# Optimization experiments

Hardware: AMD Instinct MI355X
Metric: run time of the kernel (lower is better)

The kernel has to match this reference:

```python
import jax, jax.numpy as jnp
import numpy as np
import math

B = 2048
INPUT_SIZE = 1024
OUTPUT_SIZE = 512
SPONGE = 1024
ACT = 256
REC = 256
STORE = ACT + REC  # 512
DEPTH = 8
BDEPTH = 10
NEUTRAL_C = 1.0
SQRT2 = math.sqrt(2.0)


def _make_structure():
    # Deterministic stand-in for the module's random.sample-based recall wiring.
    rng = np.random.RandomState(0)
    half = (SPONGE + 1) // 2
    shuffle_perm = np.array([i // 2 + (i % 2) * half for i in range(SPONGE)], dtype=np.int64)
    unused = []
    recall = []
    for i in range(DEPTH):
        unused.extend(range(i * STORE, (i + 1) * STORE))
        sel = rng.choice(len(unused), size=REC, replace=False)
        sel_set = set(sel.tolist())
        recall.append([unused[k] for k in sorted(sel_set)])
        unused = [u for k, u in enumerate(unused) if k not in sel_set]
    out_mem = np.array(sorted(unused), dtype=np.int64)  # 2048 leftover memory columns
    bf_size = len(out_mem) + SPONGE  # 3072
    bf_depth = int(math.ceil(math.log2(bf_size)))  # 12
    bf_half = (bf_size + 1) // 2
    bf_perm = np.array([i // 2 + (i % 2) * bf_half for i in range(bf_size)], dtype=np.int64)
    return shuffle_perm, np.array(recall, dtype=np.int64), out_mem, bf_perm, bf_size, bf_depth


def setup_inputs() -> dict:
    key = jax.random.key(0)
    ks = jax.random.split(key, 6)
    shuffle_perm, recall_idx, out_mem_idx, bf_perm, bf_size, bf_depth = _make_structure()
    return {
        "X": jax.random.normal(ks[0], (B, INPUT_SIZE), jnp.float32),
        "scales": jnp.ones((INPUT_SIZE,), jnp.float32),
        "angles": jax.random.uniform(ks[1], (DEPTH, BDEPTH, SPONGE // 2), jnp.float32) * (2 * math.pi),
        "act_bias": jax.random.normal(ks[2], (DEPTH, ACT), jnp.float32),
        "act_activation": jax.random.normal(ks[3], (DEPTH, ACT), jnp.float32),
        "act_curvature": jax.random.normal(ks[4], (DEPTH, ACT), jnp.float32),
        "bf_angles": jax.random.uniform(ks[5], (bf_depth, bf_size // 2), jnp.float32) * (2 * math.pi),
        "shuffle_perm": jnp.asarray(shuffle_perm),
        "recall_idx": jnp.asarray(recall_idx),
        "output_mem_idx": jnp.asarray(out_mem_idx),
        "bf_perm": jnp.asarray(bf_perm),
    }


def _base_activation(x, c):
    # In the source, `a` is overwritten with torch.tensor(1.0), so a == 1.
    t = (math.pi / 4) / c
    y0 = (1.0 / c) * (1.0 / SQRT2 - math.cos(math.pi / 2))  # = 1/(c*sqrt(2))
    m0 = math.sin(math.pi / 2)  # = 1
    y1 = (1.0 / c) * (1.0 / SQRT2 - 1.0)
    m1 = math.sin(0.0)  # = 0
    mid = (1.0 / c) * (1.0 / SQRT2 - jnp.cos(math.pi / 4 + c * x))
    return jnp.where(x > t, y0 + m0 * (x - t), jnp.where(x < -t, y1 + m1 * (x + t), mid))


def _butterfly(x, angles, perm):
    # angles: [n_layers, exch]; shuffle -> Givens rotation per pair, extra passthrough
    exch = angles.shape[1]
    for j in range(angles.shape[0]):
        s = x[:, perm]
        x1, x2 = s[:, :exch], s[:, exch:2 * exch]
        ca, sa = jnp.cos(angles[j]), jnp.sin(angles[j])
        x = jnp.concatenate([ca * x1 + sa * x2, -sa * x1 + ca * x2, s[:, 2 * exch:]], axis=1)
    return x


def reference(X, scales, angles, act_bias, act_activation, act_curvature, bf_angles,
              shuffle_perm, recall_idx, output_mem_idx, bf_perm):
    Xs = X * scales
    sponge = Xs[:, :SPONGE]  # input_size == sponge_size: no zero pad, memory[0] is empty
    mem = jnp.zeros((Xs.shape[0], DEPTH * STORE), Xs.dtype)
    for i in range(DEPTH):
        sponge = _butterfly(sponge, angles[i], shuffle_perm)
        x1 = sponge[:, STORE:STORE + ACT] + act_bias[i]  # activation_position == store_size
        c = 0.5 * NEUTRAL_C * (act_curvature[i] + jnp.sqrt(act_curvature[i] ** 2 + 1.0))
        ap = _base_activation(x1, c)
        am = _base_activation(-x1, c)
        act_out = jnp.stack([ap, am], axis=2).reshape(ap.shape[0], 2 * ACT)  # interleave +/-
        mem = mem.at[:, i * STORE:(i + 1) * STORE].set(sponge[:, :STORE])
        recall = mem[:, recall_idx[i]]  # indices only address already-filled columns
        # [act_out | sponge[store:act_pos] (empty) | sponge[act_pos+ACT:] | recall]
        sponge = jnp.concatenate([act_out, sponge[:, STORE + ACT:], recall], axis=1)
    pre = jnp.concatenate([mem[:, output_mem_idx], sponge], axis=1)  # [B, 3072]
    out = _butterfly(pre, bf_angles, bf_perm)
    return out[:, :OUTPUT_SIZE]
```

## Files before the change

### kernel.cpp

```cpp
#include <hip/hip_runtime.h>
#include <math.h>

#define NB 2048
#define DEPTH 8

#define FTAB_OFF    0
#define BF01_OFF    81920
#define BFF_OFF     88064
#define ACT4_OFF    98304
#define PHYSA_OFF   106496
#define PHYSR_OFF   110592
#define PHYSO2_OFF  112640

#define MB0 2304
#define MB1 3328

#define SBAR() asm volatile("s_waitcnt lgkmcnt(0)\n\ts_barrier" ::: "memory")

__global__ void setup_kernel(const float* __restrict__ angles,
                             const float* __restrict__ bf_angles,
                             const float* __restrict__ act_bias,
                             const float* __restrict__ act_curv,
                             const int* __restrict__ recall_idx,
                             const int* __restrict__ out_mem_idx,
                             float* __restrict__ ws) {
    __shared__ int physL[4096];
    __shared__ int rcl[2048];
    __shared__ int oml[2048];
    if (blockIdx.x < 200) {
        int id = blockIdx.x * 256 + threadIdx.x;
        if (id < 40960) {
            int w = id & 3, t = (id >> 2) & 255, dg = id >> 10;
            int d = dg / 5, g = dg - 5 * d;
            int a = 2 * (t & 127) + (t >> 7);
            int pair = (w == 0) ? a : (w == 1) ? (a + 256)
                     : (w == 2) ? (2 * a) : (2 * a + 1);
            int st = 2 * g + (w >> 1);
            float ang = angles[(d * 10 + st) * 512 + pair];
            float s, c; __sincosf(ang, &s, &c);
            ws[FTAB_OFF + 2 * id]     = c;
            ws[FTAB_OFF + 2 * id + 1] = s;
        } else if (id < 44032) {
            int e = id - 40960;
            int w = e & 3; int ti = e >> 2;
            int t = ti / 3; int i = ti - 3 * t;
            int a = t + 256 * i;
            int pair = (w == 0) ? a : (w == 1) ? (a + 768)
                     : (w == 2) ? (2 * a) : (2 * a + 1);
            int stage = (w < 2) ? 0 : 1;
            float ang = bf_angles[stage * 1536 + pair];
            float s, c; __sincosf(ang, &s, &c);
            ws[BF01_OFF + 2 * e]     = c;
            ws[BF01_OFF + 2 * e + 1] = s;
        } else if (id < 49152) {
            int e = id - 44032;
            int f = e >> 10; int rem = e & 1023; int t = rem >> 2; int w = rem & 3;
            int P;
            if (f == 0) P = 3 * t;
            else if (f < 4) { int k = 8 - 2 * f;
                              P = ((t >> (2 * f)) * (768 >> k)) + (t & ((256 >> k) - 1)); }
            else P = t;
            int pair = (w == 0) ? P : (w == 1) ? (P + 768)
                     : (w == 2) ? (2 * P) : (2 * P + 1);
            int stage = (w < 2) ? (2 + 2 * f) : (3 + 2 * f);
            float ang = bf_angles[stage * 1536 + pair];
            float s, c; __sincosf(ang, &s, &c);
            ws[BFF_OFF + 2 * e]     = c;
            ws[BFF_OFF + 2 * e + 1] = s;
        } else if (id < 51200) {
            int ida = id - 49152;
            float cu = act_curv[ida];
            float c  = 0.5f * (cu + sqrtf(cu * cu + 1.0f));
            ((float4*)(ws + ACT4_OFF))[ida] =
                make_float4(act_bias[ida], c, 1.0f / c, 0.0f);
        }
    } else {
        int tid = threadIdx.x;
        for (int e = tid; e < 2048; e += 256) rcl[e] = recall_idx[e];
        for (int e = tid; e < 2048; e += 256) oml[e] = out_mem_idx[e];
        for (int e = tid; e < 512; e += 256) physL[e] = e;
        __syncthreads();
        for (int d = 1; d < 8; ++d) {
            for (int j = tid; j < 512; j += 256) {
                int p;
                if (j < 256) p = 256 + d * 256 + j;
                else          p = physL[rcl[(d - 1) * 256 + (j - 256)]];
                physL[512 * d + j] = p;
            }
            __syncthreads();
        }
        int* pa = (int*)(ws + PHYSA_OFF);
        for (int e = tid; e < 2048; e += 256) {
            int d = e >> 8, t = e & 255;
            int a = 2 * (t & 127) + (t >> 7);
            pa[2 * e]     = physL[d * 512 + 2 * a];
            pa[2 * e + 1] = physL[d * 512 + 2 * a + 1];
        }
        int* pr = (int*)(ws + PHYSR_OFF);
        for (int e = tid; e < 2048; e += 256)
            pr[e] = physL[rcl[e]];
        int* po = (int*)(ws + PHYSO2_OFF);
        for (int e = tid; e < 3072; e += 256) {
            int tt = e / 12; int r = e - 12 * tt; int i = r >> 2; int k = r & 3;
            int a = tt + 256 * i;
            int tl2 = a >> 1, th2 = a & 1;
            int pos = tl2 + 1536 * th2 + 384 * k;
            po[e] = (pos < 2048) ? physL[oml[pos]]
                                 : MB0 + (pos - 2048);
        }
    }
}

__device__ __forceinline__ float actf(float x, float c, float ic) {
    const float is2 = 0.70710678118654752f;
    float tt = 0.78539816339744831f * ic;
    float y0 = is2 * ic;
    float y1 = (is2 - 1.0f) * ic;
    float mid = ic * (is2 - __cosf(0.78539816339744831f + c * x));
    return x > tt ? (y0 + (x - tt)) : (x < -tt ? y1 : mid);
}

__launch_bounds__(256, 8)
__global__ void sponge_kernel(const float* __restrict__ X,
                              const float* __restrict__ scales,
                              const float* __restrict__ ws,
                              float* __restrict__ out) {
    __shared__ float L[4352];
    const int t = threadIdx.x;
    const int row = blockIdx.x;

    const float4* bf01  = (const float4*)(ws + BF01_OFF);
    const float4* bff   = (const float4*)(ws + BFF_OFF);
    const float4* act4  = (const float4*)(ws + ACT4_OFF);
    const int2* physA  = (const int2*)(ws + PHYSA_OFF);
    const int*  physr  = (const int*)(ws + PHYSR_OFF);
    const int*  physo2 = (const int*)(ws + PHYSO2_OFF);

    const int tl = t & 127, th = t >> 7;
    const int b  = tl + th * 512;
    const int a  = 2 * tl + th;
    const int Wn = 2 * (tl & 15) + 32 * th + 64 * (tl >> 4);
    const int Rn = (tl & 1) + 2 * ((tl >> 2) & 15) + 32 * ((tl >> 1) & 1)
                 + 64 * (tl >> 6) + 512 * th;
    const int u  = t - 128;

    float h0, h1, h2, h3;
    {
        const float* Xr = X + (size_t)row * 1024;
        h0 = Xr[b]       * scales[b];
        h1 = Xr[b + 128] * scales[b + 128];
        h2 = Xr[b + 256] * scales[b + 256];
        h3 = Xr[b + 384] * scales[b + 384];
    }

    int woff = MB0, roff = MB1;
    const float4* ft = (const float4*)(ws + FTAB_OFF) + 2 * t;
    float4 csA = ft[0], csB = ft[1];

#define DQUAD(cA, cB, i0, i1, i2, i3, F0, F1, F2, F3)                    \
    { float g0 =  (cA).x * (i0) + (cA).y * (i2);                         \
      float g2 = -(cA).y * (i0) + (cA).x * (i2);                         \
      float g1 =  (cA).z * (i1) + (cA).w * (i3);                         \
      float g3 = -(cA).w * (i1) + (cA).z * (i3);                         \
      F0 =  (cB).x * g0 + (cB).y * g1;                                   \
      F2 = -(cB).y * g0 + (cB).x * g1;                                   \
      F1 =  (cB).z * g2 + (cB).w * g3;                                   \
      F3 = -(cB).w * g2 + (cB).z * g3; }

    for (int d = 0; d < DEPTH; ++d) {
        for (int g = 0; g < 5; ++g) {
            float f0, f1, f2, f3;
            DQUAD(csA, csB, h0, h1, h2, h3, f0, f1, f2, f3);
            if (g < 4) {
                *(float2*)(L + woff + Wn)       = make_float2(f0, f1);
                *(float2*)(L + woff + Wn + 512) = make_float2(f2, f3);
                { int tmp = woff; woff = roff; roff = tmp; }
                ft += 512;
                float4 nA = ft[0], nB = ft[1];
                SBAR();
                h0 = L[roff + Rn];
                h1 = L[roff + Rn + 128];
                h2 = L[roff + Rn + 256];
                h3 = L[roff + Rn + 384];
                csA = nA; csB = nB;
            } else {
                int2 pm = physA[d * 256 + t];
                L[pm.x] = f0;
                L[pm.y] = f1;
                *(float2*)(L + woff + 2 * a) = make_float2(f2, f3);
                { int tmp = woff; woff = roff; roff = tmp; }
                ft += 512;
                float4 nA = ft[0], nB = ft[1];
                int r0 = 0, r1 = 0;
                float4 a0, a1, a2, a3;
                if (t < 128) {
                    int k0 = t >> 1;
                    a0 = act4[d * 256 + k0];
                    a1 = act4[d * 256 + k0 + 64];
                    a2 = act4[d * 256 + k0 + 128];
                    a3 = act4[d * 256 + k0 + 192];
                } else {
                    r0 = physr[d * 256 + u];
                    r1 = physr[d * 256 + u + 128];
                }
                SBAR();
                const float* Z = L + roff;
                if (t < 128) {
                    int k0 = t >> 1;
                    float sgn = (t & 1) ? -1.0f : 1.0f;
                    float z0 = Z[k0];
                    float z1 = Z[k0 + 64];
                    float z2 = Z[k0 + 128];
                    float z3 = Z[k0 + 192];
                    h0 = actf(sgn * (z0 + a0.x), a0.y, a0.z);
                    h1 = actf(sgn * (z1 + a1.x), a1.y, a1.z);
                    h2 = actf(sgn * (z2 + a2.x), a2.y, a2.z);
                    h3 = actf(sgn * (z3 + a3.x), a3.y, a3.z);
                } else {
                    h0 = Z[256 + u];
                    h1 = Z[384 + u];
                    h2 = L[r0];
                    h3 = L[r1];
                }
                csA = nA; csB = nB;
            }
        }
    }

    int4 pg0, pg1, pg2;
    {
        const int4* pgp = (const int4*)(physo2 + t * 12);
        pg0 = pgp[0]; pg1 = pgp[1]; pg2 = pgp[2];
    }
    L[MB0 + b]       = h0;
    L[MB0 + b + 128] = h1;
    L[MB0 + b + 256] = h2;
    L[MB0 + b + 384] = h3;
    SBAR();

    float w0, w1, w2, w3, w4, w5, w6, w7, w8, w9, w10, w11;
    w0 = L[pg0.x]; w1 = L[pg0.y]; w2 = L[pg0.z]; w3 = L[pg0.w];
    w4 = L[pg1.x]; w5 = L[pg1.y]; w6 = L[pg1.z]; w7 = L[pg1.w];
    w8 = L[pg2.x]; w9 = L[pg2.y]; w10 = L[pg2.z]; w11 = L[pg2.w];
    SBAR();

#define BF01_STEP(i, q0, q1, q2, q3)                                     \
    {                                                                    \
        float4 c01 = bf01[(t * 3 + (i)) * 2];                            \
        float4 c23 = bf01[(t * 3 + (i)) * 2 + 1];                        \
        float y0, y1, y2, y3;                                            \
        DQUAD(c01, c23, q0, q1, q2, q3, y0, y1, y2, y3);                 \
        *(float2*)(L + 2 * t + 512 * (i))        = make_float2(y0, y1);  \
        *(float2*)(L + 2 * t + 512 * (i) + 1536) = make_float2(y2, y3);  \
    }
    BF01_STEP(0, w0, w1, w2, w3)
    BF01_STEP(1, w4, w5, w6, w7)
    BF01_STEP(2, w8, w9, w10, w11)
#undef BF01_STEP
    SBAR();

#pragma unroll
    for (int f = 0; f < 4; ++f) {
        int P;
        if (f == 0) P = 3 * t;
        else { const int k = 8 - 2 * f;
               P = ((t >> (2 * f)) * (768 >> k)) + (t & ((256 >> k) - 1)); }
        int base = (P >> 1) + (P & 1) * 1536;
        float4 csS = bff[(f * 256 + t) * 2];
        float4 csT = bff[(f * 256 + t) * 2 + 1];
        float x1p = L[base];
        float x1q = L[base + 384];
        float x2p = L[base + 768];
        float x2q = L[base + 1152];
        float o1P =  csS.x * x1p + csS.y * x2p;
        float o2P = -csS.y * x1p + csS.x * x2p;
        float o1Q =  csS.z * x1q + csS.w * x2q;
        float o2Q = -csS.w * x1q + csS.z * x2q;
        float y0 =  csT.x * o1P + csT.y * o1Q;
        float y2 = -csT.y * o1P + csT.x * o1Q;
        float y1 =  csT.z * o2P + csT.w * o2Q;
        float y3 = -csT.w * o2P + csT.z * o2Q;
        SBAR();
        *(float2*)(L + 2 * P)        = make_float2(y0, y1);
        *(float2*)(L + 2 * P + 1536) = make_float2(y2, y3);
        SBAR();
    }

    {
        int base = (t >> 1) + (t & 1) * 1536;
        float4 csS = bff[(4 * 256 + t) * 2];
        float4 csT = bff[(4 * 256 + t) * 2 + 1];
        float x1p = L[base];
        float x1q = L[base + 384];
        float x2p = L[base + 768];
        float x2q = L[base + 1152];
        float o1P =  csS.x * x1p + csS.y * x2p;
        float o2P = -csS.y * x1p + csS.x * x2p;
        float o1Q =  csS.z * x1q + csS.w * x2q;
        float o2Q = -csS.w * x1q + csS.z * x2q;
        *(float2*)(out + (size_t)row * 512 + 2 * t) =
            make_float2(csT.x * o1P + csT.y * o1Q, csT.z * o2P + csT.w * o2Q);
    }
#undef DQUAD
}

extern "C" void kernel_launch(void* const* d_in, const int* in_sizes, int n_in,
                              void* d_out, int out_size, void* d_ws, size_t ws_size,
                              hipStream_t stream) {
    const float* X          = (const float*)d_in[0];
    const float* scales     = (const float*)d_in[1];
    const float* angles     = (const float*)d_in[2];
    const float* act_bias   = (const float*)d_in[3];
    const float* act_curv   = (const float*)d_in[5];
    const float* bf_angles  = (const float*)d_in[6];
    const int*   recall_idx  = (const int*)d_in[8];
    const int*   out_mem_idx = (const int*)d_in[9];

    float* ws = (float*)d_ws;

    setup_kernel<<<201, 256, 0, stream>>>(angles, bf_angles, act_bias, act_curv,
                                          recall_idx, out_mem_idx, ws);
    sponge_kernel<<<NB, 256, 0, stream>>>(X, scales, ws, (float*)d_out);
}
```

Measured before the change: 123.5 us.

## Halve threads per row and give each thread two butterfly quads

```diff
diff --git a/kernel.cpp b/kernel.cpp
--- a/kernel.cpp
+++ b/kernel.cpp
@@ -12,8 +12,8 @@
 #define PHYSR_OFF   110592
 #define PHYSO2_OFF  112640
 
-#define MB0 2304
-#define MB1 3328
+#define EXB  2304
+#define EXB1 3328
 
 #define SBAR() asm volatile("s_waitcnt lgkmcnt(0)\n\ts_barrier" ::: "memory")
 
@@ -106,7 +106,7 @@
             int tl2 = a >> 1, th2 = a & 1;
             int pos = tl2 + 1536 * th2 + 384 * k;
             po[e] = (pos < 2048) ? physL[oml[pos]]
-                                 : MB0 + (pos - 2048);
+                                 : EXB + (pos - 2048);
         }
     }
 }
@@ -120,7 +120,7 @@
     return x > tt ? (y0 + (x - tt)) : (x < -tt ? y1 : mid);
 }
 
-__launch_bounds__(256, 8)
+__launch_bounds__(128, 4)
 __global__ void sponge_kernel(const float* __restrict__ X,
                               const float* __restrict__ scales,
                               const float* __restrict__ ws,
@@ -136,26 +136,19 @@
     const int*  physr  = (const int*)(ws + PHYSR_OFF);
     const int*  physo2 = (const int*)(ws + PHYSO2_OFF);
 
-    const int tl = t & 127, th = t >> 7;
-    const int b  = tl + th * 512;
-    const int a  = 2 * tl + th;
-    const int Wn = 2 * (tl & 15) + 32 * th + 64 * (tl >> 4);
-    const int Rn = (tl & 1) + 2 * ((tl >> 2) & 15) + 32 * ((tl >> 1) & 1)
-                 + 64 * (tl >> 6) + 512 * th;
-    const int u  = t - 128;
-
-    float h0, h1, h2, h3;
+    const int WX = 4 * (t & 15) + 128 * (t >> 4);
+    const int RX = 2 * ((t & 1) + 2 * ((t >> 2) & 15) + 32 * ((t >> 1) & 1)
+                      + 64 * (t >> 6));
+
+    float h0[4], h1[4];
     {
         const float* Xr = X + (size_t)row * 1024;
-        h0 = Xr[b]       * scales[b];
-        h1 = Xr[b + 128] * scales[b + 128];
-        h2 = Xr[b + 256] * scales[b + 256];
-        h3 = Xr[b + 384] * scales[b + 384];
-    }
-
-    int woff = MB0, roff = MB1;
-    const float4* ft = (const float4*)(ws + FTAB_OFF) + 2 * t;
-    float4 csA = ft[0], csB = ft[1];
+#pragma unroll
+        for (int m = 0; m < 4; ++m) {
+            h0[m] = Xr[t + 128 * m]       * scales[t + 128 * m];
+            h1[m] = Xr[t + 512 + 128 * m] * scales[t + 512 + 128 * m];
+        }
+    }
 
 #define DQUAD(cA, cB, i0, i1, i2, i3, F0, F1, F2, F3)                    \
     { float g0 =  (cA).x * (i0) + (cA).y * (i2);                         \
@@ -167,139 +160,169 @@
       F1 =  (cB).z * g2 + (cB).w * g3;                                   \
       F3 = -(cB).w * g2 + (cB).z * g3; }
 
+    int woff = EXB, roff = EXB1;
+    const float4* ft = (const float4*)(ws + FTAB_OFF) + 2 * t;
+    float4 cA0 = ft[0], cB0 = ft[1];
+    float4 cA1 = ft[256], cB1 = ft[257];
+    int4 pg0a, pg0b, pg0c, pg1a, pg1b, pg1c;
+
     for (int d = 0; d < DEPTH; ++d) {
-        for (int g = 0; g < 5; ++g) {
-            float f0, f1, f2, f3;
-            DQUAD(csA, csB, h0, h1, h2, h3, f0, f1, f2, f3);
-            if (g < 4) {
-                *(float2*)(L + woff + Wn)       = make_float2(f0, f1);
-                *(float2*)(L + woff + Wn + 512) = make_float2(f2, f3);
-                { int tmp = woff; woff = roff; roff = tmp; }
-                ft += 512;
-                float4 nA = ft[0], nB = ft[1];
-                SBAR();
-                h0 = L[roff + Rn];
-                h1 = L[roff + Rn + 128];
-                h2 = L[roff + Rn + 256];
-                h3 = L[roff + Rn + 384];
-                csA = nA; csB = nB;
-            } else {
-                int2 pm = physA[d * 256 + t];
-                L[pm.x] = f0;
-                L[pm.y] = f1;
-                *(float2*)(L + woff + 2 * a) = make_float2(f2, f3);
-                { int tmp = woff; woff = roff; roff = tmp; }
-                ft += 512;
-                float4 nA = ft[0], nB = ft[1];
-                int r0 = 0, r1 = 0;
-                float4 a0, a1, a2, a3;
-                if (t < 128) {
-                    int k0 = t >> 1;
-                    a0 = act4[d * 256 + k0];
-                    a1 = act4[d * 256 + k0 + 64];
-                    a2 = act4[d * 256 + k0 + 128];
-                    a3 = act4[d * 256 + k0 + 192];
-                } else {
-                    r0 = physr[d * 256 + u];
-                    r1 = physr[d * 256 + u + 128];
-                }
-                SBAR();
-                const float* Z = L + roff;
-                if (t < 128) {
-                    int k0 = t >> 1;
-                    float sgn = (t & 1) ? -1.0f : 1.0f;
-                    float z0 = Z[k0];
-                    float z1 = Z[k0 + 64];
-                    float z2 = Z[k0 + 128];
-                    float z3 = Z[k0 + 192];
-                    h0 = actf(sgn * (z0 + a0.x), a0.y, a0.z);
-                    h1 = actf(sgn * (z1 + a1.x), a1.y, a1.z);
-                    h2 = actf(sgn * (z2 + a2.x), a2.y, a2.z);
-                    h3 = actf(sgn * (z3 + a3.x), a3.y, a3.z);
-                } else {
-                    h0 = Z[256 + u];
-                    h1 = Z[384 + u];
-                    h2 = L[r0];
-                    h3 = L[r1];
-                }
-                csA = nA; csB = nB;
+        float4 a0, a1, a2, a3;
+        int r0 = 0, r1 = 0;
+        int2 pm0, pm1;
+#pragma unroll
+        for (int g = 0; g < 4; ++g) {
+            float f00, f01, f02, f03, f10, f11, f12, f13;
+            DQUAD(cA0, cB0, h0[0], h0[1], h0[2], h0[3], f00, f01, f02, f03);
+            DQUAD(cA1, cB1, h1[0], h1[1], h1[2], h1[3], f10, f11, f12, f13);
+            *(float4*)(L + woff + WX)      = make_float4(f00, f02, f01, f03);
+            *(float4*)(L + woff + WX + 64) = make_float4(f10, f12, f11, f13);
+            { int tmp = woff; woff = roff; roff = tmp; }
+            ft += 512;
+            float4 nA0 = ft[0], nB0 = ft[1];
+            float4 nA1 = ft[256], nB1 = ft[257];
+            if (g == 2) { pm0 = physA[d * 256 + t]; pm1 = physA[d * 256 + t + 128]; }
+            if (g == 3) {
+                int k0 = t >> 1;
+                a0 = act4[d * 256 + k0];       a1 = act4[d * 256 + k0 + 64];
+                a2 = act4[d * 256 + k0 + 128]; a3 = act4[d * 256 + k0 + 192];
+                r0 = physr[d * 256 + t];       r1 = physr[d * 256 + t + 128];
             }
-        }
-    }
-
-    int4 pg0, pg1, pg2;
+            SBAR();
+            float2 e0 = *(const float2*)(L + roff + RX);
+            float2 e1 = *(const float2*)(L + roff + RX + 256);
+            float2 e2 = *(const float2*)(L + roff + RX + 512);
+            float2 e3 = *(const float2*)(L + roff + RX + 768);
+            h0[0] = e0.x; h1[0] = e0.y; h0[1] = e1.x; h1[1] = e1.y;
+            h0[2] = e2.x; h1[2] = e2.y; h0[3] = e3.x; h1[3] = e3.y;
+            cA0 = nA0; cB0 = nB0; cA1 = nA1; cB1 = nB1;
+        }
+        {
+            float f00, f01, f02, f03, f10, f11, f12, f13;
+            DQUAD(cA0, cB0, h0[0], h0[1], h0[2], h0[3], f00, f01, f02, f03);
+            DQUAD(cA1, cB1, h1[0], h1[1], h1[2], h1[3], f10, f11, f12, f13);
+            L[pm0.x] = f00; L[pm0.y] = f01;
+            L[pm1.x] = f10; L[pm1.y] = f11;
+            *(float4*)(L + woff + 4 * t) = make_float4(f02, f03, f12, f13);
+            { int tmp = woff; woff = roff; roff = tmp; }
+            ft += 512;
+            float4 nA0 = ft[0], nB0 = ft[1];
+            float4 nA1 = ft[256], nB1 = ft[257];
+            if (d == DEPTH - 1) {
+                const int4* p0 = (const int4*)(physo2 + t * 12);
+                const int4* p1 = (const int4*)(physo2 + (t + 128) * 12);
+                pg0a = p0[0]; pg0b = p0[1]; pg0c = p0[2];
+                pg1a = p1[0]; pg1b = p1[1]; pg1c = p1[2];
+            }
+            SBAR();
+            const float* Z = L + roff;
+            int k0 = t >> 1;
+            float sgn = (t & 1) ? -1.0f : 1.0f;
+            h0[0] = actf(sgn * (Z[k0]       + a0.x), a0.y, a0.z);
+            h0[1] = actf(sgn * (Z[k0 + 64]  + a1.x), a1.y, a1.z);
+            h0[2] = actf(sgn * (Z[k0 + 128] + a2.x), a2.y, a2.z);
+            h0[3] = actf(sgn * (Z[k0 + 192] + a3.x), a3.y, a3.z);
+            h1[0] = Z[256 + t]; h1[1] = Z[384 + t];
+            h1[2] = L[r0];      h1[3] = L[r1];
+            cA0 = nA0; cB0 = nB0; cA1 = nA1; cB1 = nB1;
+        }
+    }
+
+    float4 c0a[3], c0b[3], c1a[3], c1b[3];
+#pragma unroll
+    for (int i = 0; i < 3; ++i) {
+        c0a[i] = bf01[(t * 3 + i) * 2];         c0b[i] = bf01[(t * 3 + i) * 2 + 1];
+        c1a[i] = bf01[((t + 128) * 3 + i) * 2]; c1b[i] = bf01[((t + 128) * 3 + i) * 2 + 1];
+    }
+#pragma unroll
+    for (int m = 0; m < 4; ++m) {
+        L[EXB + t + 128 * m]       = h0[m];
+        L[EXB + 512 + t + 128 * m] = h1[m];
+    }
+    SBAR();
+
+    float w0[12], w1[12];
+    w0[0] = L[pg0a.x]; w0[1] = L[pg0a.y]; w0[2]  = L[pg0a.z]; w0[3]  = L[pg0a.w];
+    w0[4] = L[pg0b.x]; w0[5] = L[pg0b.y]; w0[6]  = L[pg0b.z]; w0[7]  = L[pg0b.w];
+    w0[8] = L[pg0c.x]; w0[9] = L[pg0c.y]; w0[10] = L[pg0c.z]; w0[11] = L[pg0c.w];
+    w1[0] = L[pg1a.x]; w1[1] = L[pg1a.y]; w1[2]  = L[pg1a.z]; w1[3]  = L[pg1a.w];
+    w1[4] = L[pg1b.x]; w1[5] = L[pg1b.y]; w1[6]  = L[pg1b.z]; w1[7]  = L[pg1b.w];
+    w1[8] = L[pg1c.x]; w1[9] = L[pg1c.y]; w1[10] = L[pg1c.z]; w1[11] = L[pg1c.w];
+    float4 cS0 = bff[t * 2],         cT0 = bff[t * 2 + 1];
+    float4 cS1 = bff[(t + 128) * 2], cT1 = bff[(t + 128) * 2 + 1];
+    SBAR();
+
+#pragma unroll
+    for (int i = 0; i < 3; ++i) {
+        float y0, y1, y2, y3;
+        DQUAD(c0a[i], c0b[i], w0[4 * i], w0[4 * i + 1], w0[4 * i + 2], w0[4 * i + 3],
+              y0, y1, y2, y3);
+        *(float2*)(L + 2 * t + 512 * i)        = make_float2(y0, y1);
+        *(float2*)(L + 2 * t + 512 * i + 1536) = make_float2(y2, y3);
+        DQUAD(c1a[i], c1b[i], w1[4 * i], w1[4 * i + 1], w1[4 * i + 2], w1[4 * i + 3],
+              y0, y1, y2, y3);
+        *(float2*)(L + 2 * t + 256 + 512 * i)        = make_float2(y0, y1);
+        *(float2*)(L + 2 * t + 256 + 512 * i + 1536) = make_float2(y2, y3);
+    }
+    SBAR();
+
+#pragma unroll
+    for (int f = 0; f < 4; ++f) {
+        int P0, P1;
+        if (f == 0) { P0 = 3 * t; P1 = 3 * (t + 128); }
+        else { const int k = 8 - 2 * f;
+               P0 = ((t >> (2 * f)) * (768 >> k)) + (t & ((256 >> k) - 1));
+               P1 = (((t + 128) >> (2 * f)) * (768 >> k)) + ((t + 128) & ((256 >> k) - 1)); }
+        int b0 = (P0 >> 1) + (P0 & 1) * 1536;
+        int b1 = (P1 >> 1) + (P1 & 1) * 1536;
+        float x10 = L[b0], x20 = L[b0 + 384], x30 = L[b0 + 768], x40 = L[b0 + 1152];
+        float x11 = L[b1], x21 = L[b1 + 384], x31 = L[b1 + 768], x41 = L[b1 + 1152];
+        float o1P =  cS0.x * x10 + cS0.y * x30;
+        float o2P = -cS0.y * x10 + cS0.x * x30;
+        float o1Q =  cS0.z * x20 + cS0.w * x40;
+        float o2Q = -cS0.w * x20 + cS0.z * x40;
+        float y00 =  cT0.x * o1P + cT0.y * o1Q;
+        float y02 = -cT0.y * o1P + cT0.x * o1Q;
+        float y01 =  cT0.z * o2P + cT0.w * o2Q;
+        float y03 = -cT0.w * o2P + cT0.z * o2Q;
+        o1P =  cS1.x * x11 + cS1.y * x31;
+        o2P = -cS1.y * x11 + cS1.x * x31;
+        o1Q =  cS1.z * x21 + cS1.w * x41;
+        o2Q = -cS1.w * x21 + cS1.z * x41;
+        float y10 =  cT1.x * o1P + cT1.y * o1Q;
+        float y12 = -cT1.y * o1P + cT1.x * o1Q;
+        float y11 =  cT1.z * o2P + cT1.w * o2Q;
+        float y13 = -cT1.w * o2P + cT1.z * o2Q;
+        float4 nS0 = bff[((f + 1) * 256 + t) * 2];
+        float4 nT0 = bff[((f + 1) * 256 + t) * 2 + 1];
+        float4 nS1 = bff[((f + 1) * 256 + t + 128) * 2];
+        float4 nT1 = bff[((f + 1) * 256 + t + 128) * 2 + 1];
+        SBAR();
+        *(float2*)(L + 2 * P0)        = make_float2(y00, y01);
+        *(float2*)(L + 2 * P0 + 1536) = make_float2(y02, y03);
+        *(float2*)(L + 2 * P1)        = make_float2(y10, y11);
+        *(float2*)(L + 2 * P1 + 1536) = make_float2(y12, y13);
+        SBAR();
+        cS0 = nS0; cT0 = nT0; cS1 = nS1; cT1 = nT1;
+    }
+
     {
-        const int4* pgp = (const int4*)(physo2 + t * 12);
-        pg0 = pgp[0]; pg1 = pgp[1]; pg2 = pgp[2];
-    }
-    L[MB0 + b]       = h0;
-    L[MB0 + b + 128] = h1;
-    L[MB0 + b + 256] = h2;
-    L[MB0 + b + 384] = h3;
-    SBAR();
-
-    float w0, w1, w2, w3, w4, w5, w6, w7, w8, w9, w10, w11;
-    w0 = L[pg0.x]; w1 = L[pg0.y]; w2 = L[pg0.z]; w3 = L[pg0.w];
-    w4 = L[pg1.x]; w5 = L[pg1.y]; w6 = L[pg1.z]; w7 = L[pg1.w];
-    w8 = L[pg2.x]; w9 = L[pg2.y]; w10 = L[pg2.z]; w11 = L[pg2.w];
-    SBAR();
-
-#define BF01_STEP(i, q0, q1, q2, q3)                                     \
-    {                                                                    \
-        float4 c01 = bf01[(t * 3 + (i)) * 2];                            \
-        float4 c23 = bf01[(t * 3 + (i)) * 2 + 1];                        \
-        float y0, y1, y2, y3;                                            \
-        DQUAD(c01, c23, q0, q1, q2, q3, y0, y1, y2, y3);                 \
-        *(float2*)(L + 2 * t + 512 * (i))        = make_float2(y0, y1);  \
-        *(float2*)(L + 2 * t + 512 * (i) + 1536) = make_float2(y2, y3);  \
-    }
-    BF01_STEP(0, w0, w1, w2, w3)
-    BF01_STEP(1, w4, w5, w6, w7)
-    BF01_STEP(2, w8, w9, w10, w11)
-#undef BF01_STEP
-    SBAR();
-
-#pragma unroll
-    for (int f = 0; f < 4; ++f) {
-        int P;
-        if (f == 0) P = 3 * t;
-        else { const int k = 8 - 2 * f;
-               P = ((t >> (2 * f)) * (768 >> k)) + (t & ((256 >> k) - 1)); }
-        int base = (P >> 1) + (P & 1) * 1536;
-        float4 csS = bff[(f * 256 + t) * 2];
-        float4 csT = bff[(f * 256 + t) * 2 + 1];
-        float x1p = L[base];
-        float x1q = L[base + 384];
-        float x2p = L[base + 768];
-        float x2q = L[base + 1152];
-        float o1P =  csS.x * x1p + csS.y * x2p;
-        float o2P = -csS.y * x1p + csS.x * x2p;
-        float o1Q =  csS.z * x1q + csS.w * x2q;
-        float o2Q = -csS.w * x1q + csS.z * x2q;
-        float y0 =  csT.x * o1P + csT.y * o1Q;
-        float y2 = -csT.y * o1P + csT.x * o1Q;
-        float y1 =  csT.z * o2P + csT.w * o2Q;
-        float y3 = -csT.w * o2P + csT.z * o2Q;
-        SBAR();
-        *(float2*)(L + 2 * P)        = make_float2(y0, y1);
-        *(float2*)(L + 2 * P + 1536) = make_float2(y2, y3);
-        SBAR();
-    }
-
-    {
-        int base = (t >> 1) + (t & 1) * 1536;
-        float4 csS = bff[(4 * 256 + t) * 2];
-        float4 csT = bff[(4 * 256 + t) * 2 + 1];
-        float x1p = L[base];
-        float x1q = L[base + 384];
-        float x2p = L[base + 768];
-        float x2q = L[base + 1152];
-        float o1P =  csS.x * x1p + csS.y * x2p;
-        float o2P = -csS.y * x1p + csS.x * x2p;
-        float o1Q =  csS.z * x1q + csS.w * x2q;
-        float o2Q = -csS.w * x1q + csS.z * x2q;
+        int b0 = (t >> 1) + (t & 1) * 1536;
+        int b1 = b0 + 64;
+        float x10 = L[b0], x20 = L[b0 + 384], x30 = L[b0 + 768], x40 = L[b0 + 1152];
+        float x11 = L[b1], x21 = L[b1 + 384], x31 = L[b1 + 768], x41 = L[b1 + 1152];
+        float o1P =  cS0.x * x10 + cS0.y * x30;
+        float o2P = -cS0.y * x10 + cS0.x * x30;
+        float o1Q =  cS0.z * x20 + cS0.w * x40;
+        float o2Q = -cS0.w * x20 + cS0.z * x40;
         *(float2*)(out + (size_t)row * 512 + 2 * t) =
-            make_float2(csT.x * o1P + csT.y * o1Q, csT.z * o2P + csT.w * o2Q);
+            make_float2(cT0.x * o1P + cT0.y * o1Q, cT0.z * o2P + cT0.w * o2Q);
+        o1P =  cS1.x * x11 + cS1.y * x31;
+        o2P = -cS1.y * x11 + cS1.x * x31;
+        o1Q =  cS1.z * x21 + cS1.w * x41;
+        o2Q = -cS1.w * x21 + cS1.z * x41;
+        *(float2*)(out + (size_t)row * 512 + 2 * t + 256) =
+            make_float2(cT1.x * o1P + cT1.y * o1Q, cT1.z * o2P + cT1.w * o2Q);
     }
 #undef DQUAD
 }
@@ -320,5 +343,5 @@
 
     setup_kernel<<<201, 256, 0, stream>>>(angles, bf_angles, act_bias, act_curv,
                                           recall_idx, out_mem_idx, ws);
-    sponge_kernel<<<NB, 256, 0, stream>>>(X, scales, ws, (float*)d_out);
+    sponge_kernel<<<NB, 128, 0, stream>>>(X, scales, ws, (float*)d_out);
 }
```

Measured after the change: 120.4 us. 1.03x faster.
